# Kernel optimization log

Hardware: AMD Instinct MI355X
Metric: run time of the kernel (lower is better)

The kernel has to match this reference:

```python
import jax
import jax.numpy as jnp
import numpy as np


def setup_inputs() -> dict:
    key = jax.random.key(0)
    k1, k2 = jax.random.split(key)
    B, C, H, W = 2, 256, 64, 128  # 1/8-res RAFT features of a 512x1024 image
    fmap1 = jax.random.normal(k1, (B, C, H, W), dtype=jnp.float32)
    fmap2 = jax.random.normal(k2, (B, C, H, W), dtype=jnp.float32)
    return {"fmap1": fmap1, "fmap2": fmap2, "k": 32}


def reference(fmap1, fmap2, k):
    B, C, H, W = fmap1.shape
    N = H * W
    f1 = fmap1.reshape(B, C, N)
    f2 = fmap2.reshape(B, C, N)

    # --- KNN (FAISS inner-product search), indices are non-differentiable ---
    scores = jnp.einsum('bcn,bcm->bnm', jax.lax.stop_gradient(f1),
                        jax.lax.stop_gradient(f2))  # [B, N1, N2]
    _, idx = jax.lax.top_k(scores, k)               # [B, N1, k]
    idx = jnp.transpose(idx, (0, 2, 1))             # [B, k, N1]

    # --- gather top-k target features: gathered[b,c,j,n] = f2[b,c,idx[b,j,n]] ---
    gathered = jax.vmap(lambda f, i: f[:, i])(f2, idx)  # [B, C, k, N1]

    # --- sparse correlation ---
    corr_sp = jnp.einsum('bcn,bckn->bkn', f1, gathered) / jnp.sqrt(jnp.float32(C))

    # --- coordinate grids (y-first), relative displacement ---
    ys, xs = jnp.meshgrid(jnp.arange(H, dtype=jnp.float32),
                          jnp.arange(W, dtype=jnp.float32), indexing='ij')
    coords = jnp.stack([ys.ravel(), xs.ravel()])          # [2, N], y first
    coords0 = jnp.broadcast_to(coords[None, :, None, :], (B, 2, k, N))
    coords1 = jnp.transpose(coords[:, idx], (1, 0, 2, 3))  # [B, 2, k, N]
    coords1 = coords1 - coords0                            # relative offsets

    batch_index = jnp.broadcast_to(
        jnp.arange(B, dtype=jnp.float32).reshape(B, 1, 1, 1), (B, 1, k, N))

    return corr_sp, coords0, coords1, batch_index
```

## Files before the change

### kernel.cpp

```cpp
#include <hip/hip_runtime.h>
#include <hip/hip_bf16.h>

#define B_  2
#define C_  256
#define H_  64
#define W_  128
#define N_  (H_ * W_)
#define K_  32
#define Q_  10
#define CK2 36
#define TN  32
#define TM  16
#define NHT 64
#define RR  16

typedef short  short8  __attribute__((ext_vector_type(8)));
typedef short  short4v __attribute__((ext_vector_type(4)));
typedef float  floatx4 __attribute__((ext_vector_type(4)));

__device__ __forceinline__ unsigned umin_(unsigned a, unsigned b) { return a < b ? a : b; }
__device__ __forceinline__ unsigned umax_(unsigned a, unsigned b) { return a > b ? a : b; }
__device__ __forceinline__ ushort f2bf(float v) {
    __hip_bfloat16 h = __float2bfloat16(v);
    ushort u; __builtin_memcpy(&u, &h, 2); return u;
}
__device__ __forceinline__ unsigned med3u(unsigned a, unsigned b, unsigned c) {
    unsigned d;
    asm("v_med3_u32 %0, %1, %2, %3" : "=v"(d) : "v"(a), "v"(b), "v"(c));
    return d;
}

__device__ __forceinline__ unsigned packkey(float v, int m) {
    const float vc = v > 0.0f ? v : 0.0f;
    unsigned b; __builtin_memcpy(&b, &vc, 4);
    return (b & 0xFFFFE000u) | (unsigned)m;
}

__device__ __forceinline__ void qinsert(unsigned (&q)[Q_], unsigned k) {
#pragma unroll
    for (int i = Q_ - 1; i > 0; --i)
        q[i] = med3u(q[i - 1], k, q[i]);
    q[0] = umax_(q[0], k);
}

#define CSWAP(a, b) { const unsigned _mx = umax_(a, b); \
                      const unsigned _mn = umin_(a, b); (a) = _mx; (b) = _mn; }

__device__ __forceinline__ void gl_lds16(const ushort* g, ushort* l) {
    __builtin_amdgcn_global_load_lds(
        (const __attribute__((address_space(1))) unsigned int*)(g),
        (__attribute__((address_space(3))) unsigned int*)(l),
        16, 0, 0);
}

__global__ void raft_prep_kernel(const float* __restrict__ f1,
                                 const float* __restrict__ f2,
                                 float* __restrict__ f1Tf,
                                 ushort* __restrict__ f2T,
                                 float* __restrict__ f2Tf) {
    __shared__ float tile[32][33];
    const int nt = blockIdx.x;
    const int ct = blockIdx.y;
    const int z  = blockIdx.z;
    const int b  = z >> 1;
    const float* __restrict__ src = (z & 1) ? f2 : f1;
    const int tid = threadIdx.x;

    {
        const int cl = tid >> 3;
        const int nx = tid & 7;
        const float4 v = *(const float4*)(
            src + ((size_t)b * C_ + (ct * 32 + cl)) * N_ + (nt * 32 + nx * 4));
        tile[cl][nx * 4 + 0] = v.x;
        tile[cl][nx * 4 + 1] = v.y;
        tile[cl][nx * 4 + 2] = v.z;
        tile[cl][nx * 4 + 3] = v.w;
    }
    __syncthreads();
    {
        const int nl = tid >> 3;
        const int c4 = (tid & 7) * 4;
        float4 v;
        v.x = tile[c4 + 0][nl];
        v.y = tile[c4 + 1][nl];
        v.z = tile[c4 + 2][nl];
        v.w = tile[c4 + 3][nl];
        const size_t o = ((size_t)b * N_ + (nt * 32 + nl)) * C_ + (ct * 32 + c4);
        if (z & 1) {
            *(float4*)(f2Tf + o) = v;
            short4v h;
            h[0] = (short)f2bf(v.x); h[1] = (short)f2bf(v.y);
            h[2] = (short)f2bf(v.z); h[3] = (short)f2bf(v.w);
            *(short4v*)(f2T + o) = h;
        } else {
            *(float4*)(f1Tf + o) = v;
        }
    }
}

__launch_bounds__(512, 4)
__global__ void raft_stage1_kernel(const float* __restrict__ f1Tf,
                                   const ushort* __restrict__ f2T,
                                   ushort* __restrict__ cand) {
    __shared__ __align__(16) ushort Bt[2][8][2048];

    const int bid0 = blockIdx.x;
    const int bid  = ((bid0 & 7) << 6) | (bid0 >> 3);
    const int b    = bid >> 8;
    const int nt0  = (bid & 255) * TN;
    const int tid  = threadIdx.x;
    const int w    = tid >> 6;
    const int lane = tid & 63;
    const int p    = lane & 15;
    const int q4   = lane >> 4;

    short8 af[2][8];
    #pragma unroll
    for (int ns = 0; ns < 2; ++ns) {
        const float* __restrict__ arow =
            f1Tf + ((size_t)b * N_ + nt0 + ns * 16 + p) * C_;
        #pragma unroll
        for (int ks = 0; ks < 8; ++ks) {
            const float4 x = *(const float4*)(arow + ks * 32 + q4 * 8);
            const float4 y = *(const float4*)(arow + ks * 32 + q4 * 8 + 4);
            short8 t;
            t[0] = (short)f2bf(x.x); t[1] = (short)f2bf(x.y);
            t[2] = (short)f2bf(x.z); t[3] = (short)f2bf(x.w);
            t[4] = (short)f2bf(y.x); t[5] = (short)f2bf(y.y);
            t[6] = (short)f2bf(y.z); t[7] = (short)f2bf(y.w);
            af[ns][ks] = t;
        }
    }

    unsigned q0[Q_], q1[Q_];
    #pragma unroll
    for (int i = 0; i < Q_; ++i) { q0[i] = 0u; q1[i] = 0u; }

    const ushort* __restrict__ f2Tb = f2T + (size_t)b * N_ * C_;
    const ushort* gsrc[4];
    #pragma unroll
    for (int i = 0; i < 4; ++i) {
        const int s  = w * 64 + i * 512 + lane;
        const int es = s >> 8;
        const int r  = (s >> 4) & 15;
        const int cc = (s & 15) ^ (r & 7);
        gsrc[i] = f2Tb + ((size_t)es * 1024 + r) * C_ + cc * 8;
    }
    const int sbase = (w * 64) * 8;

    #pragma unroll
    for (int i = 0; i < 4; ++i)
        gl_lds16(gsrc[i], &Bt[0][0][0] + sbase + i * 512 * 8);
    __syncthreads();

    floatx4 acc0, acc1;
    for (int mt = 0; mt < NHT; ++mt) {
        {
            const size_t off = (size_t)mt * TM * C_ + 128;
            #pragma unroll
            for (int i = 0; i < 4; ++i)
                gl_lds16(gsrc[i] + off, &Bt[1][0][0] + sbase + i * 512 * 8);
        }
        acc0 = (floatx4){0.f, 0.f, 0.f, 0.f};
        acc1 = (floatx4){0.f, 0.f, 0.f, 0.f};
        {
            const ushort* __restrict__ cur = &Bt[0][w][0];
            #pragma unroll
            for (int ks = 0; ks < 4; ++ks) {
                const int c = ks * 4 + q4;
                const short8 bm = *(const short8*)(&cur[(p * 16 + (c ^ (p & 7))) * 8]);
                acc0 = __builtin_amdgcn_mfma_f32_16x16x32_bf16(bm, af[0][ks], acc0, 0, 0, 0);
                acc1 = __builtin_amdgcn_mfma_f32_16x16x32_bf16(bm, af[1][ks], acc1, 0, 0, 0);
            }
        }
        __syncthreads();

        if (mt + 1 < NHT) {
            const size_t off = (size_t)(mt + 1) * TM * C_;
            #pragma unroll
            for (int i = 0; i < 4; ++i)
                gl_lds16(gsrc[i] + off, &Bt[0][0][0] + sbase + i * 512 * 8);
        }
        {
            const ushort* __restrict__ cur = &Bt[1][w][0];
            #pragma unroll
            for (int ks = 0; ks < 4; ++ks) {
                const int c = ks * 4 + q4;
                const short8 bm = *(const short8*)(&cur[(p * 16 + (c ^ (p & 7))) * 8]);
                acc0 = __builtin_amdgcn_mfma_f32_16x16x32_bf16(bm, af[0][4 + ks], acc0, 0, 0, 0);
                acc1 = __builtin_amdgcn_mfma_f32_16x16x32_bf16(bm, af[1][4 + ks], acc1, 0, 0, 0);
            }
        }

        const int mb = w * 1024 + mt * TM + q4 * 4;
        {
            unsigned k0 = packkey(acc0[0], mb + 0);
            unsigned k1 = packkey(acc0[1], mb + 1);
            unsigned k2 = packkey(acc0[2], mb + 2);
            unsigned k3 = packkey(acc0[3], mb + 3);
            CSWAP(k0, k1); CSWAP(k2, k3); CSWAP(k0, k2); CSWAP(k1, k3); CSWAP(k1, k2);
            qinsert(q0, k0);
            if (__any(k1 > q0[Q_ - 1])) {
                qinsert(q0, k1);
                if (__any(k2 > q0[Q_ - 1])) {
                    qinsert(q0, k2);
                    if (__any(k3 > q0[Q_ - 1])) qinsert(q0, k3);
                }
            }
        }
        {
            unsigned k0 = packkey(acc1[0], mb + 0);
            unsigned k1 = packkey(acc1[1], mb + 1);
            unsigned k2 = packkey(acc1[2], mb + 2);
            unsigned k3 = packkey(acc1[3], mb + 3);
            CSWAP(k0, k1); CSWAP(k2, k3); CSWAP(k0, k2); CSWAP(k1, k3); CSWAP(k1, k2);
            qinsert(q1, k0);
            if (__any(k1 > q1[Q_ - 1])) {
                qinsert(q1, k1);
                if (__any(k2 > q1[Q_ - 1])) {
                    qinsert(q1, k2);
                    if (__any(k3 > q1[Q_ - 1])) qinsert(q1, k3);
                }
            }
        }
        __syncthreads();
    }

    unsigned* __restrict__ smem = (unsigned*)&Bt[0][0][0];
    const int qi = w * 4 + q4;
    #pragma unroll
    for (int t = 0; t < Q_; ++t) {
        smem[(qi * Q_ + t) * 33 + p]      = q0[t];
        smem[(qi * Q_ + t) * 33 + 16 + p] = q1[t];
    }
    __syncthreads();

    unsigned* __restrict__ ms = smem + 10560;
    if (tid < 128) {
        const int r = tid >> 2, g = tid & 3;
        const int lb = g * 8;
        int i0 = 0, i1 = 0, i2 = 0, i3 = 0, i4 = 0, i5 = 0, i6 = 0, i7 = 0;
        for (int t = 0; t < CK2; ++t) {
            const unsigned a0 = (i0 < Q_) ? smem[((lb + 0) * Q_ + i0) * 33 + r] : 0u;
            const unsigned a1 = (i1 < Q_) ? smem[((lb + 1) * Q_ + i1) * 33 + r] : 0u;
            const unsigned a2 = (i2 < Q_) ? smem[((lb + 2) * Q_ + i2) * 33 + r] : 0u;
            const unsigned a3 = (i3 < Q_) ? smem[((lb + 3) * Q_ + i3) * 33 + r] : 0u;
            const unsigned a4 = (i4 < Q_) ? smem[((lb + 4) * Q_ + i4) * 33 + r] : 0u;
            const unsigned a5 = (i5 < Q_) ? smem[((lb + 5) * Q_ + i5) * 33 + r] : 0u;
            const unsigned a6 = (i6 < Q_) ? smem[((lb + 6) * Q_ + i6) * 33 + r] : 0u;
            const unsigned a7 = (i7 < Q_) ? smem[((lb + 7) * Q_ + i7) * 33 + r] : 0u;
            const unsigned mx = umax_(umax_(umax_(a0, a1), umax_(a2, a3)),
                                      umax_(umax_(a4, a5), umax_(a6, a7)));
            ms[(g * CK2 + t) * 33 + r] = mx;
            const bool e0 = (a0 == mx);
            const bool e1 = !e0 && (a1 == mx);
            const bool e2 = !e0 && !e1 && (a2 == mx);
            const bool e3 = !e0 && !e1 && !e2 && (a3 == mx);
            const bool e4 = !e0 && !e1 && !e2 && !e3 && (a4 == mx);
            const bool e5 = !e0 && !e1 && !e2 && !e3 && !e4 && (a5 == mx);
            const bool e6 = !e0 && !e1 && !e2 && !e3 && !e4 && !e5 && (a6 == mx);
            const bool e7 = !e0 && !e1 && !e2 && !e3 && !e4 && !e5 && !e6 && (a7 == mx);
            i0 += e0; i1 += e1; i2 += e2; i3 += e3;
            i4 += e4; i5 += e5; i6 += e6; i7 += e7;
        }
    }
    __syncthreads();

    if (tid < 32) {
        int i0 = 0, i1 = 0, i2 = 0, i3 = 0;
        ushort* __restrict__ myc = cand + ((size_t)(b * N_ + nt0 + tid)) * CK2;
        for (int t = 0; t < CK2; ++t) {
            const unsigned a0 = ms[(0 * CK2 + i0) * 33 + tid];
            const unsigned a1 = ms[(1 * CK2 + i1) * 33 + tid];
            const unsigned a2 = ms[(2 * CK2 + i2) * 33 + tid];
            const unsigned a3 = ms[(3 * CK2 + i3) * 33 + tid];
            const unsigned m01 = umax_(a0, a1), m23 = umax_(a2, a3);
            const unsigned mx  = umax_(m01, m23);
            myc[t] = (ushort)(mx & 0x1FFFu);
            i0 += (a0 == mx);
            i1 += (a0 != mx) & (a1 == mx);
            i2 += (a0 != mx) & (a1 != mx) & (a2 == mx);
            i3 += (a0 != mx) & (a1 != mx) & (a2 != mx) & (a3 == mx);
        }
    }
}

__launch_bounds__(576)
__global__ void raft_rerank_kernel(const float* __restrict__ f1Tf,
                                   const float* __restrict__ f2Tf,
                                   const ushort* __restrict__ cand,
                                   float* __restrict__ out) {
    __shared__ float  aS[RR][C_];
    __shared__ float  cs[RR][CK2];
    __shared__ ushort cmS[RR][CK2];
    const int bid0 = blockIdx.x;
    const int bid  = ((bid0 & 7) << 7) | (bid0 >> 3);
    const int row0 = bid * RR;
    const int tid  = threadIdx.x;
    const int r    = tid / CK2;
    const int c    = tid - r * CK2;

    for (int sidx = tid; sidx < RR * (C_ / 4); sidx += RR * CK2) {
        const int rr = sidx >> 6, s4 = sidx & 63;
        const int rg = row0 + rr;
        const int bb = rg >> 13, nn = rg & (N_ - 1);
        *(float4*)(&aS[rr][s4 * 4]) =
            *(const float4*)(f1Tf + ((size_t)bb * N_ + nn) * C_ + s4 * 4);
    }
    cmS[r][c] = cand[(size_t)(row0 + r) * CK2 + c];
    __syncthreads();

    {
        const int rg = row0 + r;
        const int bb = rg >> 13;
        const int m  = cmS[r][c];
        const float* __restrict__ bRow = f2Tf + ((size_t)bb * N_ + m) * C_;
        float acc = 0.0f;
        for (int c4 = 0; c4 < C_; c4 += 4) {
            const float4 b4 = *(const float4*)(bRow + c4);
            acc = fmaf(aS[r][c4 + 0], b4.x, acc);
            acc = fmaf(aS[r][c4 + 1], b4.y, acc);
            acc = fmaf(aS[r][c4 + 2], b4.z, acc);
            acc = fmaf(aS[r][c4 + 3], b4.w, acc);
        }
        cs[r][c] = acc;
    }
    __syncthreads();

    const int rg = row0 + r;
    const int bb = rg >> 13;
    const int n  = rg & (N_ - 1);
    const int y0 = n >> 7, x0 = n & 127;
    {
        const float v = cs[r][c];
        const int m = cmS[r][c];
        int rank = 0;
        for (int j = 0; j < CK2; ++j) {
            const float vj = cs[r][j];
            rank += (vj > v) || ((vj == v) && (cmS[r][j] < m));
        }
        if (rank < K_) {
            const size_t posn = (size_t)rank * N_ + n;
            out[(size_t)bb * (K_ * N_) + posn] = v * 0.0625f;
            const size_t c1b = (size_t)1572864 + (size_t)bb * 2 * K_ * N_;
            out[c1b + posn]                     = (float)((m >> 7) - y0);
            out[c1b + (size_t)(K_ * N_) + posn] = (float)((m & 127) - x0);
        }
    }
    if (c < K_) {
        const size_t posn = (size_t)c * N_ + n;
        const size_t c0b = (size_t)524288 + (size_t)bb * 2 * K_ * N_;
        out[c0b + posn]                     = (float)y0;
        out[c0b + (size_t)(K_ * N_) + posn] = (float)x0;
        out[(size_t)2621440 + (size_t)bb * (K_ * N_) + posn] = (float)bb;
    }
}

extern "C" void kernel_launch(void* const* d_in, const int* in_sizes, int n_in,
                              void* d_out, int out_size, void* d_ws, size_t ws_size,
                              hipStream_t stream) {
    const float* f1 = (const float*)d_in[0];
    const float* f2 = (const float*)d_in[1];

    float*  f1Tf = (float*)d_ws;
    float*  f2Tf = f1Tf + (size_t)B_ * N_ * C_;
    ushort* f2T  = (ushort*)(f2Tf + (size_t)B_ * N_ * C_);
    ushort* cand = f2T + (size_t)B_ * N_ * C_;

    raft_prep_kernel<<<dim3(N_ / 32, C_ / 32, B_ * 2), dim3(256), 0, stream>>>(
        f1, f2, f1Tf, f2T, f2Tf);

    raft_stage1_kernel<<<dim3(B_ * (N_ / TN)), dim3(512), 0, stream>>>(f1Tf, f2T, cand);

    raft_rerank_kernel<<<dim3(B_ * N_ / RR), dim3(RR * CK2), 0, stream>>>(
        f1Tf, f2Tf, cand, (float*)d_out);
}
```

Baseline: 323.5 us.

## Bucket rerank candidate pairs by target region to improve f2 cache locality

```diff
diff --git a/kernel.cpp b/kernel.cpp
--- a/kernel.cpp
+++ b/kernel.cpp
@@ -13,6 +13,7 @@
 #define TM  16
 #define NHT 64
 #define RR  16
+#define BCAP 40960
 
 typedef short  short8  __attribute__((ext_vector_type(8)));
 typedef short  short4v __attribute__((ext_vector_type(4)));
@@ -285,13 +286,81 @@
     }
 }
 
+__global__ void raft_zero_kernel(unsigned* __restrict__ gcnt) {
+    if (threadIdx.x < 16) gcnt[threadIdx.x] = 0u;
+}
+
+__launch_bounds__(256)
+__global__ void raft_scatter_kernel(const ushort* __restrict__ cand,
+                                    unsigned* __restrict__ pairs,
+                                    unsigned* __restrict__ gcnt) {
+    __shared__ unsigned h[16], base[16];
+    const int bid = blockIdx.x;
+    const int tid = threadIdx.x;
+    const int row = bid * 64 + (tid >> 2);
+    const int j0  = (tid & 3) * 9;
+    const int bb  = row >> 13;
+    if (tid < 16) h[tid] = 0u;
+    __syncthreads();
+    ushort mloc[9];
+    #pragma unroll
+    for (int u = 0; u < 9; ++u) {
+        const ushort m = cand[(size_t)row * CK2 + j0 + u];
+        mloc[u] = m;
+        atomicAdd(&h[bb * 8 + (m >> 10)], 1u);
+    }
+    __syncthreads();
+    if (tid < 16) { base[tid] = atomicAdd(&gcnt[tid], h[tid]); h[tid] = 0u; }
+    __syncthreads();
+    #pragma unroll
+    for (int u = 0; u < 9; ++u) {
+        const int bkt = bb * 8 + (mloc[u] >> 10);
+        const unsigned idx = base[bkt] + atomicAdd(&h[bkt], 1u);
+        pairs[(size_t)bkt * BCAP + idx] = ((unsigned)row << 6) | (unsigned)(j0 + u);
+    }
+}
+
+__launch_bounds__(256)
+__global__ void raft_score_kernel(const float* __restrict__ f1Tf,
+                                  const float* __restrict__ f2Tf,
+                                  const ushort* __restrict__ cand,
+                                  const unsigned* __restrict__ pairs,
+                                  const unsigned* __restrict__ gcnt,
+                                  float* __restrict__ cs) {
+    const int bid = blockIdx.x;
+    const int mt  = bid & 7;
+    const int bb  = (bid >> 3) & 1;
+    const int sl  = bid >> 4;
+    const int bkt = bb * 8 + mt;
+    const unsigned cnt = umin_(gcnt[bkt], (unsigned)BCAP);
+    const unsigned lo = (cnt * (unsigned)sl) >> 6;
+    const unsigned hi = (cnt * (unsigned)(sl + 1)) >> 6;
+    const unsigned* __restrict__ pb = pairs + (size_t)bkt * BCAP;
+    for (unsigned i = lo + threadIdx.x; i < hi; i += 256) {
+        const unsigned pid = pb[i];
+        const unsigned row = pid >> 6;
+        const unsigned j   = pid & 63;
+        const int m = cand[(size_t)row * CK2 + j];
+        const float* __restrict__ aRow = f1Tf + (size_t)row * C_;
+        const float* __restrict__ bRow = f2Tf + ((size_t)bb * N_ + m) * C_;
+        float acc = 0.0f;
+        for (int c4 = 0; c4 < C_; c4 += 4) {
+            const float4 a4 = *(const float4*)(aRow + c4);
+            const float4 b4 = *(const float4*)(bRow + c4);
+            acc = fmaf(a4.x, b4.x, acc);
+            acc = fmaf(a4.y, b4.y, acc);
+            acc = fmaf(a4.z, b4.z, acc);
+            acc = fmaf(a4.w, b4.w, acc);
+        }
+        cs[(size_t)row * CK2 + j] = acc;
+    }
+}
+
 __launch_bounds__(576)
-__global__ void raft_rerank_kernel(const float* __restrict__ f1Tf,
-                                   const float* __restrict__ f2Tf,
-                                   const ushort* __restrict__ cand,
-                                   float* __restrict__ out) {
-    __shared__ float  aS[RR][C_];
-    __shared__ float  cs[RR][CK2];
+__global__ void raft_rank_kernel(const ushort* __restrict__ cand,
+                                 const float* __restrict__ cs,
+                                 float* __restrict__ out) {
+    __shared__ float  csS[RR][CK2];
     __shared__ ushort cmS[RR][CK2];
     const int bid0 = blockIdx.x;
     const int bid  = ((bid0 & 7) << 7) | (bid0 >> 3);
@@ -300,31 +369,8 @@
     const int r    = tid / CK2;
     const int c    = tid - r * CK2;
 
-    for (int sidx = tid; sidx < RR * (C_ / 4); sidx += RR * CK2) {
-        const int rr = sidx >> 6, s4 = sidx & 63;
-        const int rg = row0 + rr;
-        const int bb = rg >> 13, nn = rg & (N_ - 1);
-        *(float4*)(&aS[rr][s4 * 4]) =
-            *(const float4*)(f1Tf + ((size_t)bb * N_ + nn) * C_ + s4 * 4);
-    }
     cmS[r][c] = cand[(size_t)(row0 + r) * CK2 + c];
-    __syncthreads();
-
-    {
-        const int rg = row0 + r;
-        const int bb = rg >> 13;
-        const int m  = cmS[r][c];
-        const float* __restrict__ bRow = f2Tf + ((size_t)bb * N_ + m) * C_;
-        float acc = 0.0f;
-        for (int c4 = 0; c4 < C_; c4 += 4) {
-            const float4 b4 = *(const float4*)(bRow + c4);
-            acc = fmaf(aS[r][c4 + 0], b4.x, acc);
-            acc = fmaf(aS[r][c4 + 1], b4.y, acc);
-            acc = fmaf(aS[r][c4 + 2], b4.z, acc);
-            acc = fmaf(aS[r][c4 + 3], b4.w, acc);
-        }
-        cs[r][c] = acc;
-    }
+    csS[r][c] = cs[(size_t)(row0 + r) * CK2 + c];
     __syncthreads();
 
     const int rg = row0 + r;
@@ -332,11 +378,11 @@
     const int n  = rg & (N_ - 1);
     const int y0 = n >> 7, x0 = n & 127;
     {
-        const float v = cs[r][c];
+        const float v = csS[r][c];
         const int m = cmS[r][c];
         int rank = 0;
         for (int j = 0; j < CK2; ++j) {
-            const float vj = cs[r][j];
+            const float vj = csS[r][j];
             rank += (vj > v) || ((vj == v) && (cmS[r][j] < m));
         }
         if (rank < K_) {
@@ -367,11 +413,21 @@
     ushort* f2T  = (ushort*)(f2Tf + (size_t)B_ * N_ * C_);
     ushort* cand = f2T + (size_t)B_ * N_ * C_;
 
+    unsigned* pairs = (unsigned*)f2T;
+    float*    cs    = (float*)((char*)f2T + 2621440);
+    unsigned* gcnt  = (unsigned*)((char*)f2T + 4980736);
+
     raft_prep_kernel<<<dim3(N_ / 32, C_ / 32, B_ * 2), dim3(256), 0, stream>>>(
         f1, f2, f1Tf, f2T, f2Tf);
 
     raft_stage1_kernel<<<dim3(B_ * (N_ / TN)), dim3(512), 0, stream>>>(f1Tf, f2T, cand);
 
-    raft_rerank_kernel<<<dim3(B_ * N_ / RR), dim3(RR * CK2), 0, stream>>>(
-        f1Tf, f2Tf, cand, (float*)d_out);
-}
+    raft_zero_kernel<<<dim3(1), dim3(64), 0, stream>>>(gcnt);
+
+    raft_scatter_kernel<<<dim3(256), dim3(256), 0, stream>>>(cand, pairs, gcnt);
+
+    raft_score_kernel<<<dim3(1024), dim3(256), 0, stream>>>(
+        f1Tf, f2Tf, cand, pairs, gcnt, cs);
+
+    raft_rank_kernel<<<dim3(1024), dim3(RR * CK2), 0, stream>>>(cand, cs, (float*)d_out);
+}
```

Result: slower. 411.6 us (+27.2%).
